# Optimization experiments

Measured on AMD Instinct MI355X. Metric: run time of the kernel, lower is better.

## Reference

```python
import jax, jax.numpy as jnp
import numpy as np

TOP_K = 4
EPS = 1e-6


def setup_inputs() -> dict:
    key = jax.random.key(0)
    k1, k2, k3 = jax.random.split(key, 3)
    B, Q, N, H, W = 4, 200, 32, 256, 256
    pred_masks = jax.random.normal(k1, (B, Q, H, W), dtype=jnp.float32)
    pred_logits = jax.random.normal(k2, (B, Q, 2), dtype=jnp.float32)
    gt_masks = (jax.random.uniform(k3, (B, N, H, W)) < 0.3).astype(jnp.float32)
    return {"pred_masks": pred_masks, "pred_logits": pred_logits, "gt_masks": gt_masks}


def _combined_scores(pred_masks, pred_logits, gt_masks):
    """IoU * class-score, shape [B, Q, N]."""
    pm = jax.nn.sigmoid(pred_masks)                    # [B,Q,H,W]
    cls = jax.nn.softmax(pred_logits, axis=-1)[..., 1]  # [B,Q]
    B, Q = pm.shape[:2]
    N = gt_masks.shape[1]
    pmf = pm.reshape(B, Q, -1)                         # [B,Q,D]
    tmf = gt_masks.reshape(B, N, -1)                   # [B,N,D]
    inter = jnp.einsum('bqd,bnd->bqn', pmf, tmf)
    union = pmf.sum(-1)[:, :, None] + tmf.sum(-1)[:, None, :] - inter
    iou = inter / (union + EPS)
    return iou * cls[:, :, None]


def _greedy_assign(combined):
    """Greedy per-GT top-k with dedup. combined: [Q,N] -> sel indices [N,k], -1 = dropped."""
    Q = combined.shape[0]
    k = min(TOP_K, Q)

    def step(assigned, col):
        _, idx = jax.lax.top_k(col, k)          # [k] query indices for this GT
        taken = assigned[idx]                   # already assigned -> drop
        sel = jnp.where(taken, -1, idx)
        assigned = assigned.at[idx].set(True)
        return assigned, sel

    _, sels = jax.lax.scan(step, jnp.zeros(Q, dtype=bool), combined.T)
    return sels  # [N, k]


def reference(pred_masks, pred_logits, gt_masks):
    combined = _combined_scores(pred_masks, pred_logits, gt_masks)  # [B,Q,N]
    sels = jax.vmap(_greedy_assign)(combined)                       # [B,N,k]
    B, N, k = sels.shape
    src_idx = sels
    tgt_idx = jnp.broadcast_to(jnp.arange(N, dtype=jnp.int32)[None, :, None], sels.shape)
    valid = sels >= 0
    tgt_idx = jnp.where(valid, tgt_idx, -1)
    return src_idx, tgt_idx, valid
```

## Files before the change

kernel.cpp:

```cpp
#include <hip/hip_runtime.h>
#include <math.h>
#include <stdint.h>

#define BB    4
#define QQ    200
#define NGT   32
#define DD    65536
#define TOPK  4
#define EPSF  1e-6f
#define QP    208

#define QT16  13
#define KG    16
#define KSPAN (DD / KG)
#define BK    256
#define NCH   (KSPAN / BK)
#define RS    260

typedef float  f32x4  __attribute__((ext_vector_type(4)));
typedef __bf16 bf16x8 __attribute__((ext_vector_type(8)));

#define GLOAD_LDS16(gp, lp)                                                       \
    __builtin_amdgcn_global_load_lds(                                             \
        (const __attribute__((address_space(1))) void*)(gp),                      \
        (__attribute__((address_space(3))) void*)(lp), 16, 0, 0)

__global__ __launch_bounds__(256) void k_pack(const float* __restrict__ gt,
                                              uint32_t* __restrict__ packed,
                                              float* __restrict__ zero_base) {
    int zidx = blockIdx.x * 256 + threadIdx.x;
    if (zidx < BB * NGT * QP + BB * QP) zero_base[zidx] = 0.0f;

    int blk = blockIdx.x;
    int b = blk >> 6;
    int d0 = ((blk & 63) * 256 + threadIdx.x) * 4;
    uint32_t px = 0, py = 0, pz = 0, pw = 0;
    const float* gb = gt + (size_t)b * NGT * DD + d0;
#pragma unroll
    for (int n = 0; n < NGT; ++n) {
        float4 g = *(const float4*)(gb + (size_t)n * DD);
        px |= (g.x > 0.5f ? 1u : 0u) << n;
        py |= (g.y > 0.5f ? 1u : 0u) << n;
        pz |= (g.z > 0.5f ? 1u : 0u) << n;
        pw |= (g.w > 0.5f ? 1u : 0u) << n;
    }
    *(uint4*)(packed + (size_t)b * DD + d0) = make_uint4(px, py, pz, pw);
}

__global__ __launch_bounds__(256) void k_tsum(const uint32_t* __restrict__ packed,
                                              float* __restrict__ tsum) {
    int b = blockIdx.x >> 5;
    int n = blockIdx.x & 31;
    const uint4* pp = (const uint4*)(packed + (size_t)b * DD);
    int cnt = 0;
    for (int i = threadIdx.x; i < DD / 4; i += 256) {
        uint4 w = pp[i];
        cnt += (int)((w.x >> n) & 1u) + (int)((w.y >> n) & 1u) +
               (int)((w.z >> n) & 1u) + (int)((w.w >> n) & 1u);
    }
#pragma unroll
    for (int off = 32; off; off >>= 1) cnt += __shfl_xor(cnt, off);
    __shared__ int red[4];
    if ((threadIdx.x & 63) == 0) red[threadIdx.x >> 6] = cnt;
    __syncthreads();
    if (threadIdx.x == 0)
        tsum[blockIdx.x] = (float)(red[0] + red[1] + red[2] + red[3]);
}

__global__ __launch_bounds__(256, 4) void k_mfma(const float* __restrict__ pm,
                                                 const uint32_t* __restrict__ packed,
                                                 float* __restrict__ inter,
                                                 float* __restrict__ psum) {
    int blk = blockIdx.x;
    int b   = blk / (QT16 * KG);
    int rem = blk % (QT16 * KG);
    int qt  = rem / KG;
    int kg  = rem % KG;
    int tid = threadIdx.x, lane = tid & 63, wave = tid >> 6;
    int m = lane & 15, quad = lane >> 4;

    __shared__ float    sA[2][16][RS];
    __shared__ uint32_t sB[2][BK];

    const size_t kbase = (size_t)kg * KSPAN;
    const float*    pmb = pm + (size_t)b * QQ * DD + kbase;
    const uint32_t* pkb = packed + (size_t)b * DD + kbase;

    auto stage = [&](int c, int bf) {
#pragma unroll
        for (int i = 0; i < 4; ++i) {
            int row = wave * 4 + i;
            int qg  = qt * 16 + row;
            int qe  = qg < QQ ? qg : QQ - 1;
            const float* gp = pmb + (size_t)qe * DD + c * BK + lane * 4;
            GLOAD_LDS16(gp, &sA[bf][row][0]);
        }
        if (wave == 0) {
            const uint32_t* gp = pkb + c * BK + lane * 4;
            GLOAD_LDS16(gp, &sB[bf][0]);
        }
    };

    f32x4 cH0 = {0.f,0.f,0.f,0.f}, cL0 = {0.f,0.f,0.f,0.f};
    f32x4 cH1 = {0.f,0.f,0.f,0.f}, cL1 = {0.f,0.f,0.f,0.f};
    float ps = 0.f;

    stage(0, 0);
    for (int c = 0; c < NCH; ++c) {
        __builtin_amdgcn_s_waitcnt(0);
        __syncthreads();
        if (c + 1 < NCH) stage(c + 1, (c + 1) & 1);
        int bf = c & 1;
#pragma unroll
        for (int st = 0; st < 2; ++st) {
            int k0 = (wave * 2 + st) * 32 + quad * 8;
            float4 a0 = *(const float4*)&sA[bf][m][k0];
            float4 a1 = *(const float4*)&sA[bf][m][k0 + 4];
            uint4  w0 = *(const uint4*)&sB[bf][k0];
            uint4  w1 = *(const uint4*)&sB[bf][k0 + 4];

            float xs[8] = {a0.x, a0.y, a0.z, a0.w, a1.x, a1.y, a1.z, a1.w};
            uint32_t hu[8], mu[8], lu[8];
#pragma unroll
            for (int i = 0; i < 8; ++i) {
                float x  = xs[i];
                float sg = __builtin_amdgcn_rcpf(1.0f + __expf(-x));
                ps += sg;
                uint32_t u0 = __float_as_uint(sg);
                float hi = __uint_as_float(u0 & 0xFFFF0000u);
                float r1 = sg - hi;
                uint32_t u1 = __float_as_uint(r1);
                float mi = __uint_as_float(u1 & 0xFFFF0000u);
                float r2 = r1 - mi;
                hu[i] = u0; mu[i] = u1; lu[i] = __float_as_uint(r2);
            }
            union { uint4 u; bf16x8 v; } ah, am, al;
            ah.u = make_uint4((hu[0] >> 16) | (hu[1] & 0xFFFF0000u),
                              (hu[2] >> 16) | (hu[3] & 0xFFFF0000u),
                              (hu[4] >> 16) | (hu[5] & 0xFFFF0000u),
                              (hu[6] >> 16) | (hu[7] & 0xFFFF0000u));
            am.u = make_uint4((mu[0] >> 16) | (mu[1] & 0xFFFF0000u),
                              (mu[2] >> 16) | (mu[3] & 0xFFFF0000u),
                              (mu[4] >> 16) | (mu[5] & 0xFFFF0000u),
                              (mu[6] >> 16) | (mu[7] & 0xFFFF0000u));
            al.u = make_uint4((lu[0] >> 16) | (lu[1] & 0xFFFF0000u),
                              (lu[2] >> 16) | (lu[3] & 0xFFFF0000u),
                              (lu[4] >> 16) | (lu[5] & 0xFFFF0000u),
                              (lu[6] >> 16) | (lu[7] & 0xFFFF0000u));

            uint32_t wj[8] = {w0.x, w0.y, w0.z, w0.w, w1.x, w1.y, w1.z, w1.w};
            union { ushort u[8]; bf16x8 v; } b0, b1;
#pragma unroll
            for (int j = 0; j < 8; ++j) {
                b0.u[j] = (ushort)((((int)(wj[j] << (31 - m))) >> 31) & 0x3F80);
                b1.u[j] = (ushort)((((int)(wj[j] << (15 - m))) >> 31) & 0x3F80);
            }

            cH0 = __builtin_amdgcn_mfma_f32_16x16x32_bf16(ah.v, b0.v, cH0, 0, 0, 0);
            cL0 = __builtin_amdgcn_mfma_f32_16x16x32_bf16(am.v, b0.v, cL0, 0, 0, 0);
            cL0 = __builtin_amdgcn_mfma_f32_16x16x32_bf16(al.v, b0.v, cL0, 0, 0, 0);
            cH1 = __builtin_amdgcn_mfma_f32_16x16x32_bf16(ah.v, b1.v, cH1, 0, 0, 0);
            cL1 = __builtin_amdgcn_mfma_f32_16x16x32_bf16(am.v, b1.v, cL1, 0, 0, 0);
            cL1 = __builtin_amdgcn_mfma_f32_16x16x32_bf16(al.v, b1.v, cL1, 0, 0, 0);
        }
    }

    ps += __shfl_xor(ps, 16);
    ps += __shfl_xor(ps, 32);
    if (lane < 16) {
        int qg = qt * 16 + m;
        if (qg < QQ) atomicAdd(&psum[b * QP + qg], ps);
    }

    float c8[8];
#pragma unroll
    for (int r = 0; r < 4; ++r) {
        c8[r]     = cH0[r] + cL0[r];
        c8[4 + r] = cH1[r] + cL1[r];
    }
    __builtin_amdgcn_s_waitcnt(0);
    __syncthreads();
    float* cred = (float*)sA;
    if (wave > 0) {
        float* dst = cred + ((wave - 1) * 64 + lane) * 9;
#pragma unroll
        for (int r = 0; r < 8; ++r) dst[r] = c8[r];
    }
    __syncthreads();
    if (wave == 0) {
#pragma unroll
        for (int wv = 0; wv < 3; ++wv) {
            const float* sp = cred + (wv * 64 + lane) * 9;
#pragma unroll
            for (int r = 0; r < 8; ++r) c8[r] += sp[r];
        }
#pragma unroll
        for (int r = 0; r < 4; ++r) {
            int qg = qt * 16 + quad * 4 + r;
            if (qg < QQ) {
                atomicAdd(&inter[(b * NGT + m) * QP + qg],      c8[r]);
                atomicAdd(&inter[(b * NGT + 16 + m) * QP + qg], c8[4 + r]);
            }
        }
    }
}

__global__ __launch_bounds__(64) void k_topk(const float* __restrict__ inter,
                                             const float* __restrict__ psum,
                                             const float* __restrict__ tsum,
                                             const float* __restrict__ logits,
                                             int* __restrict__ idx4) {
    int bn = blockIdx.x;
    int b  = bn >> 5;
    int lane = threadIdx.x;
    float tsn = tsum[bn];
    float v[4];
#pragma unroll
    for (int s = 0; s < 4; ++s) {
        int q = lane + 64 * s;
        if (q < QQ) {
            float iv = inter[(size_t)bn * QP + q];
            float un = psum[b * QP + q] + tsn - iv;
            float l0 = logits[(b * QQ + q) * 2];
            float l1 = logits[(b * QQ + q) * 2 + 1];
            float cl = 1.0f / (1.0f + expf(l0 - l1));
            v[s] = iv / (un + EPSF) * cl;
        } else {
            v[s] = -INFINITY;
        }
    }
    for (int k = 0; k < TOPK; ++k) {
        float bv = -INFINITY;
        int   bi = 0x7fffffff;
#pragma unroll
        for (int s = 0; s < 4; ++s)
            if (v[s] > bv) { bv = v[s]; bi = lane + 64 * s; }
#pragma unroll
        for (int off = 32; off; off >>= 1) {
            float ov = __shfl_xor(bv, off);
            int   oi = __shfl_xor(bi, off);
            if (ov > bv || (ov == bv && oi < bi)) { bv = ov; bi = oi; }
        }
        if (lane == (bi & 63)) v[bi >> 6] = -INFINITY;
        if (lane == 0) idx4[bn * TOPK + k] = bi;
    }
}

__global__ __launch_bounds__(64) void k_final(const int* __restrict__ idx4,
                                              int* __restrict__ out) {
    int b = blockIdx.x;
    int lane = threadIdx.x;
    int* src = out;
    int* tgt = out + BB * NGT * TOPK;
    int* val = out + 2 * BB * NGT * TOPK;
    int asg = 0;
    for (int n = 0; n < NGT; ++n) {
        int4 id = *(const int4*)&idx4[(b * NGT + n) * TOPK];
        int ids[4] = {id.x, id.y, id.z, id.w};
        int newasg = asg;
#pragma unroll
        for (int k = 0; k < TOPK; ++k) {
            int idx = ids[k];
            int owner = idx & 63, slot = idx >> 6;
            int oasg = __shfl(asg, owner);
            int taken = (oasg >> slot) & 1;
            if (lane == owner) newasg |= (1 << slot);
            if (lane == 0) {
                int o = (b * NGT + n) * TOPK + k;
                src[o] = taken ? -1 : idx;
                tgt[o] = taken ? -1 : n;
                val[o] = taken ? 0 : 1;
            }
        }
        asg = newasg;
    }
}

extern "C" void kernel_launch(void* const* d_in, const int* in_sizes, int n_in,
                              void* d_out, int out_size, void* d_ws, size_t ws_size,
                              hipStream_t stream) {
    const float* pred_masks  = (const float*)d_in[0];
    const float* pred_logits = (const float*)d_in[1];
    const float* gt_masks    = (const float*)d_in[2];

    uint8_t* ws = (uint8_t*)d_ws;
    uint32_t* packed = (uint32_t*)ws;
    float* tsum  = (float*)(ws + (size_t)BB * DD * 4);
    float* inter = tsum + BB * NGT;
    float* psum  = inter + BB * NGT * QP;
    int*   idx4  = (int*)(psum + BB * QP);

    k_pack <<<BB * (DD / 1024), 256, 0, stream>>>(gt_masks, packed, inter);
    k_tsum <<<BB * NGT,         256, 0, stream>>>(packed, tsum);
    k_mfma <<<BB * QT16 * KG,   256, 0, stream>>>(pred_masks, packed, inter, psum);
    k_topk <<<BB * NGT,          64, 0, stream>>>(inter, psum, tsum, pred_logits, idx4);
    k_final<<<BB,                64, 0, stream>>>(idx4, (int*)d_out);
}
```

Before: 354.1 us.

## Replace async LDS DMA double-buffer with register-staged prefetch and larger K chunk

The MFMA kernel no longer uses global_load_lds double buffering. It now prefetches the next chunk into registers while computing on a single LDS buffer, then writes the registers to LDS between raw barriers. The K chunk doubles to 512, which halves the number of barrier iterations. The trade-offs are more VGPR pressure from the 8 float4 prefetch registers, a single-buffer LDS hazard that relies on hand-written s_barrier and lgkmcnt waits, and possibly lower occupancy.

```diff
diff --git a/kernel.cpp b/kernel.cpp
--- a/kernel.cpp
+++ b/kernel.cpp
@@ -13,17 +13,15 @@
 #define QT16  13
 #define KG    16
 #define KSPAN (DD / KG)
-#define BK    256
+#define BK    512
 #define NCH   (KSPAN / BK)
-#define RS    260
+#define RS    516
 
 typedef float  f32x4  __attribute__((ext_vector_type(4)));
 typedef __bf16 bf16x8 __attribute__((ext_vector_type(8)));
 
-#define GLOAD_LDS16(gp, lp)                                                       \
-    __builtin_amdgcn_global_load_lds(                                             \
-        (const __attribute__((address_space(1))) void*)(gp),                      \
-        (__attribute__((address_space(3))) void*)(lp), 16, 0, 0)
+#define RAW_BARRIER() asm volatile("s_barrier" ::: "memory")
+#define LGKM_DRAIN()  asm volatile("s_waitcnt lgkmcnt(0)" ::: "memory")
 
 __global__ __launch_bounds__(256) void k_pack(const float* __restrict__ gt,
                                               uint32_t* __restrict__ packed,
@@ -79,45 +77,62 @@
     int tid = threadIdx.x, lane = tid & 63, wave = tid >> 6;
     int m = lane & 15, quad = lane >> 4;
 
-    __shared__ float    sA[2][16][RS];
-    __shared__ uint32_t sB[2][BK];
-
-    const size_t kbase = (size_t)kg * KSPAN;
-    const float*    pmb = pm + (size_t)b * QQ * DD + kbase;
-    const uint32_t* pkb = packed + (size_t)b * DD + kbase;
-
-    auto stage = [&](int c, int bf) {
-#pragma unroll
-        for (int i = 0; i < 4; ++i) {
-            int row = wave * 4 + i;
-            int qg  = qt * 16 + row;
-            int qe  = qg < QQ ? qg : QQ - 1;
-            const float* gp = pmb + (size_t)qe * DD + c * BK + lane * 4;
-            GLOAD_LDS16(gp, &sA[bf][row][0]);
-        }
-        if (wave == 0) {
-            const uint32_t* gp = pkb + c * BK + lane * 4;
-            GLOAD_LDS16(gp, &sB[bf][0]);
-        }
-    };
+    __shared__ float    sA[16][RS];
+    __shared__ uint32_t sBw[BK];
+
+    const float*    pmb = pm + (size_t)b * QQ * DD + (size_t)kg * KSPAN;
+    const uint32_t* pkb = packed + (size_t)b * DD + (size_t)kg * KSPAN;
+
+    int row0 = wave * 4;
+    int qrow[4];
+#pragma unroll
+    for (int i = 0; i < 4; ++i) {
+        int qg = qt * 16 + row0 + i;
+        qrow[i] = qg < QQ ? qg : QQ - 1;
+    }
+
+    float4 ra[8];
+    uint2  rb;
+
+#pragma unroll
+    for (int i = 0; i < 4; ++i) {
+        const float* rp = pmb + (size_t)qrow[i] * DD + lane * 4;
+        ra[2 * i]     = *(const float4*)(rp);
+        ra[2 * i + 1] = *(const float4*)(rp + 256);
+    }
+    rb = *(const uint2*)(pkb + tid * 2);
+#pragma unroll
+    for (int i = 0; i < 4; ++i) {
+        *(float4*)&sA[row0 + i][lane * 4]       = ra[2 * i];
+        *(float4*)&sA[row0 + i][256 + lane * 4] = ra[2 * i + 1];
+    }
+    *(uint2*)&sBw[tid * 2] = rb;
+    LGKM_DRAIN();
+    RAW_BARRIER();
 
     f32x4 cH0 = {0.f,0.f,0.f,0.f}, cL0 = {0.f,0.f,0.f,0.f};
     f32x4 cH1 = {0.f,0.f,0.f,0.f}, cL1 = {0.f,0.f,0.f,0.f};
     float ps = 0.f;
 
-    stage(0, 0);
     for (int c = 0; c < NCH; ++c) {
-        __builtin_amdgcn_s_waitcnt(0);
-        __syncthreads();
-        if (c + 1 < NCH) stage(c + 1, (c + 1) & 1);
-        int bf = c & 1;
-#pragma unroll
-        for (int st = 0; st < 2; ++st) {
-            int k0 = (wave * 2 + st) * 32 + quad * 8;
-            float4 a0 = *(const float4*)&sA[bf][m][k0];
-            float4 a1 = *(const float4*)&sA[bf][m][k0 + 4];
-            uint4  w0 = *(const uint4*)&sB[bf][k0];
-            uint4  w1 = *(const uint4*)&sB[bf][k0 + 4];
+        if (c + 1 < NCH) {
+            const float* base = pmb + (size_t)(c + 1) * BK;
+#pragma unroll
+            for (int i = 0; i < 4; ++i) {
+                const float* rp = base + (size_t)qrow[i] * DD + lane * 4;
+                ra[2 * i]     = *(const float4*)(rp);
+                ra[2 * i + 1] = *(const float4*)(rp + 256);
+            }
+            rb = *(const uint2*)(pkb + (size_t)(c + 1) * BK + tid * 2);
+        }
+
+#pragma unroll
+        for (int st = 0; st < 4; ++st) {
+            int k0 = (wave * 4 + st) * 32 + quad * 8;
+            float4 a0 = *(const float4*)&sA[m][k0];
+            float4 a1 = *(const float4*)&sA[m][k0 + 4];
+            uint4  w0 = *(const uint4*)&sBw[k0];
+            uint4  w1 = *(const uint4*)&sBw[k0 + 4];
 
             float xs[8] = {a0.x, a0.y, a0.z, a0.w, a1.x, a1.y, a1.z, a1.w};
             uint32_t hu[8], mu[8], lu[8];
@@ -163,6 +178,18 @@
             cL1 = __builtin_amdgcn_mfma_f32_16x16x32_bf16(am.v, b1.v, cL1, 0, 0, 0);
             cL1 = __builtin_amdgcn_mfma_f32_16x16x32_bf16(al.v, b1.v, cL1, 0, 0, 0);
         }
+
+        RAW_BARRIER();
+        if (c + 1 < NCH) {
+#pragma unroll
+            for (int i = 0; i < 4; ++i) {
+                *(float4*)&sA[row0 + i][lane * 4]       = ra[2 * i];
+                *(float4*)&sA[row0 + i][256 + lane * 4] = ra[2 * i + 1];
+            }
+            *(uint2*)&sBw[tid * 2] = rb;
+            LGKM_DRAIN();
+        }
+        RAW_BARRIER();
     }
 
     ps += __shfl_xor(ps, 16);
@@ -178,7 +205,6 @@
         c8[r]     = cH0[r] + cL0[r];
         c8[4 + r] = cH1[r] + cL1[r];
     }
-    __builtin_amdgcn_s_waitcnt(0);
     __syncthreads();
     float* cred = (float*)sA;
     if (wave > 0) {
```

After: 352.8 us. About the same (-0.4%).
